# Kernel optimization log

Measured on AMD Instinct MI355X. Metric: run time of the kernel, lower is better.

The kernel has to match this reference:

```python
import jax, jax.numpy as jnp
import numpy as np

VIS_DIM, TXT_DIM, HID = 2048, 1024, 1024


def setup_inputs() -> dict:
    key = jax.random.key(0)
    ks = jax.random.split(key, 8)
    def lin(kw, kb, fan_in, fan_out):
        bound = 1.0 / np.sqrt(fan_in)
        W = jax.random.uniform(kw, (fan_out, fan_in), jnp.float32, -bound, bound)
        b = jax.random.uniform(kb, (fan_out,), jnp.float32, -bound, bound)
        return W, b
    Wv, bv = lin(ks[0], ks[1], VIS_DIM, HID)
    Wt, bt = lin(ks[2], ks[3], TXT_DIM, HID)
    Wa, ba = lin(ks[4], ks[5], HID, 1)
    return {
        "visual_features": jax.random.normal(ks[6], (128, 256, VIS_DIM), jnp.float32),
        "text_features": jax.random.normal(ks[7], (128, TXT_DIM), jnp.float32),
        "Wv": Wv, "bv": bv, "Wt": Wt, "bt": bt, "Wa": Wa, "ba": ba,
    }


def reference(visual_features, text_features, Wv, bv, Wt, bt, Wa, ba):
    # v: (B, R, H); t: (B, 1, H) broadcast over regions
    v = jnp.einsum("brd,hd->brh", visual_features, Wv) + bv
    t = (text_features @ Wt.T + bt)[:, None, :]
    combined = jnp.tanh(v + t)                       # (B, R, H)
    scores = jnp.einsum("brh,h->br", combined, Wa[0]) + ba[0]  # (B, R)
    attention_weights = jax.nn.softmax(scores, axis=1)
    attended = jnp.einsum("br,brd->bd", attention_weights, visual_features)
    return attended, attention_weights
```

## Files before the change

kernel.cpp:

```cpp
#include <hip/hip_runtime.h>
#include <hip/hip_bf16.h>

#define VIS_DIM 2048
#define TXT_DIM 1024
#define HID     1024
#define NB      128
#define NR      256
#define M_TOT   (NB*NR)

typedef __attribute__((ext_vector_type(4))) float  f32x4;
typedef __attribute__((ext_vector_type(8))) short  short8;
typedef __attribute__((ext_vector_type(4))) unsigned short u16x4;

static __device__ __forceinline__ unsigned short f2bf(float f) {
    union { __hip_bfloat16 h; unsigned short u; } c;
    c.h = __float2bfloat16(f);
    return c.u;
}

static __device__ __forceinline__ float tanh_fast(float x) {
    float xc = fminf(fmaxf(x, -15.f), 15.f);
    float e  = __expf(2.f * xc);
    return (e - 1.f) / (e + 1.f);
}

__global__ void init_ws(float* __restrict__ scores, float* __restrict__ tbuf,
                        const float* __restrict__ bt) {
    int i = blockIdx.x * 256 + threadIdx.x;
    if (i < M_TOT) scores[i] = 0.f;
    tbuf[i] = bt[i & (HID - 1)];
}

__global__ __launch_bounds__(256) void gemm_text(const float* __restrict__ text,
                                                 const float* __restrict__ Wt,
                                                 float* __restrict__ tbuf) {
    __shared__ float As[128][33];
    __shared__ float Bs[32][33];
    const int n0  = blockIdx.x * 32;
    const int k0  = blockIdx.y * 256;
    const int tid = threadIdx.x;
    const int tm  = tid >> 3;
    const int tn  = tid & 7;
    float acc[4][4] = {};
    for (int kt = 0; kt < 8; ++kt) {
        const int k = k0 + kt * 32;
        {
            int row = tid >> 1, off = (tid & 1) * 16;
            const float* src = text + row * TXT_DIM + k + off;
            #pragma unroll
            for (int j = 0; j < 4; ++j) {
                f32x4 v = *(const f32x4*)(src + j * 4);
                As[row][off + j*4 + 0] = v.x; As[row][off + j*4 + 1] = v.y;
                As[row][off + j*4 + 2] = v.z; As[row][off + j*4 + 3] = v.w;
            }
        }
        {
            int row = tid >> 3, off = (tid & 7) * 4;
            f32x4 v = *(const f32x4*)(Wt + (size_t)(n0 + row) * TXT_DIM + k + off);
            Bs[row][off + 0] = v.x; Bs[row][off + 1] = v.y;
            Bs[row][off + 2] = v.z; Bs[row][off + 3] = v.w;
        }
        __syncthreads();
        #pragma unroll
        for (int kk = 0; kk < 32; ++kk) {
            float a[4], b[4];
            #pragma unroll
            for (int i = 0; i < 4; ++i) a[i] = As[tm*4 + i][kk];
            #pragma unroll
            for (int j = 0; j < 4; ++j) b[j] = Bs[tn*4 + j][kk];
            #pragma unroll
            for (int i = 0; i < 4; ++i)
                #pragma unroll
                for (int j = 0; j < 4; ++j) acc[i][j] += a[i] * b[j];
        }
        __syncthreads();
    }
    #pragma unroll
    for (int i = 0; i < 4; ++i)
        #pragma unroll
        for (int j = 0; j < 4; ++j)
            atomicAdd(&tbuf[(tm*4 + i) * HID + n0 + tn*4 + j], acc[i][j]);
}

#define BK 32
#define NT (VIS_DIM / BK)

static __device__ __forceinline__ int tile_off(int row, int kElem) {
    return row * 64 + (((kElem >> 3) ^ ((row >> 1) & 3)) << 4);
}

__global__ __launch_bounds__(256, 2) void gemm_vis(
        const float* __restrict__ A,
        const float* __restrict__ Bv,
        const float* __restrict__ bv,
        const float* __restrict__ wa,
        const float* __restrict__ tbuf,
        float* __restrict__ scores) {
    __shared__ __align__(16) char lds[32768];

    const int wg   = blockIdx.x;
    const int xcd  = wg & 7;
    const int loc  = wg >> 3;
    const int mb   = xcd * 32 + (loc >> 3);
    const int nb   = loc & 7;
    const int brow = mb * 128;
    const int bcol = nb * 128;

    const int tid  = threadIdx.x;
    const int lane = tid & 63;
    const int wid  = tid >> 6;
    const int wr   = wid >> 1, wc = wid & 1;

    const int srow = tid >> 3;
    const int sfs  = tid & 7;
    unsigned va0 = ((unsigned)(brow + srow      ) * VIS_DIM + sfs * 4) * 4u;
    unsigned va1 = va0 + 32u * VIS_DIM * 4u;
    unsigned va2 = va0 + 64u * VIS_DIM * 4u;
    unsigned va3 = va0 + 96u * VIS_DIM * 4u;
    unsigned vb0 = ((unsigned)(bcol + srow      ) * VIS_DIM + sfs * 4) * 4u;
    unsigned vb1 = vb0 + 32u * VIS_DIM * 4u;
    unsigned vb2 = vb0 + 64u * VIS_DIM * 4u;
    unsigned vb3 = vb0 + 96u * VIS_DIM * 4u;

    int wbyte[4];
    #pragma unroll
    for (int r = 0; r < 4; ++r) {
        int row = srow + 32 * r;
        wbyte[r] = row * 64 + (((sfs >> 1) ^ ((row >> 1) & 3)) << 4) + (sfs & 1) * 8;
    }

    f32x4 sA0, sA1, sA2, sA3, sB0, sB1, sB2, sB3;
    f32x4 tA0, tA1, tA2, tA3, tB0, tB1, tB2, tB3;
    f32x4 acc[4][4] = {};

#define GLOAD_SET(dA0,dA1,dA2,dA3,dB0,dB1,dB2,dB3)                             \
    do {                                                                       \
        asm volatile("global_load_dwordx4 %0, %1, %2"                          \
                     : "=&v"(dA0) : "v"(va0), "s"(A) : "memory");              \
        asm volatile("global_load_dwordx4 %0, %1, %2"                          \
                     : "=&v"(dA1) : "v"(va1), "s"(A) : "memory");              \
        asm volatile("global_load_dwordx4 %0, %1, %2"                          \
                     : "=&v"(dA2) : "v"(va2), "s"(A) : "memory");              \
        asm volatile("global_load_dwordx4 %0, %1, %2"                          \
                     : "=&v"(dA3) : "v"(va3), "s"(A) : "memory");              \
        asm volatile("global_load_dwordx4 %0, %1, %2"                          \
                     : "=&v"(dB0) : "v"(vb0), "s"(Bv) : "memory");             \
        asm volatile("global_load_dwordx4 %0, %1, %2"                          \
                     : "=&v"(dB1) : "v"(vb1), "s"(Bv) : "memory");             \
        asm volatile("global_load_dwordx4 %0, %1, %2"                          \
                     : "=&v"(dB2) : "v"(vb2), "s"(Bv) : "memory");             \
        asm volatile("global_load_dwordx4 %0, %1, %2"                          \
                     : "=&v"(dB3) : "v"(vb3), "s"(Bv) : "memory");             \
        va0 += BK * 4; va1 += BK * 4; va2 += BK * 4; va3 += BK * 4;            \
        vb0 += BK * 4; vb1 += BK * 4; vb2 += BK * 4; vb3 += BK * 4;            \
    } while (0)

#define GLOAD_S() GLOAD_SET(sA0,sA1,sA2,sA3,sB0,sB1,sB2,sB3)
#define GLOAD_T() GLOAD_SET(tA0,tA1,tA2,tA3,tB0,tB1,tB2,tB3)

#define VWAIT(N)                                                               \
    do {                                                                       \
        __builtin_amdgcn_sched_barrier(0);                                     \
        asm volatile("s_waitcnt vmcnt(" #N ")" ::: "memory");                  \
        __builtin_amdgcn_sched_barrier(0);                                     \
    } while (0)

#define BARRIER()                                                              \
    do {                                                                       \
        __builtin_amdgcn_sched_barrier(0);                                     \
        asm volatile("s_waitcnt lgkmcnt(0)" ::: "memory");                     \
        __builtin_amdgcn_s_barrier();                                          \
        __builtin_amdgcn_sched_barrier(0);                                     \
    } while (0)

#define CVT8(dst, v0)                                                          \
    do {                                                                       \
        u16x4 t_;                                                              \
        t_.x = f2bf((v0).x); t_.y = f2bf((v0).y);                              \
        t_.z = f2bf((v0).z); t_.w = f2bf((v0).w);                              \
        dst = t_;                                                              \
    } while (0)

#define LWRITE_SET(bufbase, dA0,dA1,dA2,dA3,dB0,dB1,dB2,dB3)                   \
    do {                                                                       \
        u16x4 w_;                                                              \
        char* la = lds + (bufbase);                                            \
        char* lb = lds + (bufbase) + 8192;                                     \
        CVT8(w_, dA0); *(u16x4*)(la + wbyte[0]) = w_;                          \
        CVT8(w_, dA1); *(u16x4*)(la + wbyte[1]) = w_;                          \
        CVT8(w_, dA2); *(u16x4*)(la + wbyte[2]) = w_;                          \
        CVT8(w_, dA3); *(u16x4*)(la + wbyte[3]) = w_;                          \
        CVT8(w_, dB0); *(u16x4*)(lb + wbyte[0]) = w_;                          \
        CVT8(w_, dB1); *(u16x4*)(lb + wbyte[1]) = w_;                          \
        CVT8(w_, dB2); *(u16x4*)(lb + wbyte[2]) = w_;                          \
        CVT8(w_, dB3); *(u16x4*)(lb + wbyte[3]) = w_;                          \
    } while (0)

#define LWRITE_S(bufbase) LWRITE_SET(bufbase, sA0,sA1,sA2,sA3,sB0,sB1,sB2,sB3)
#define LWRITE_T(bufbase) LWRITE_SET(bufbase, tA0,tA1,tA2,tA3,tB0,tB1,tB2,tB3)

#define COMPUTE(bufbase)                                                       \
    do {                                                                       \
        short8 af[4], bf[4];                                                   \
        const int kk = (lane >> 4) * 8;                                        \
        const char* la = lds + (bufbase);                                      \
        const char* lb = lds + (bufbase) + 8192;                               \
        _Pragma("unroll")                                                      \
        for (int m = 0; m < 4; ++m)                                            \
            af[m] = *(const short8*)(la + tile_off(wr*64 + m*16 + (lane&15), kk)); \
        _Pragma("unroll")                                                      \
        for (int n = 0; n < 4; ++n)                                            \
            bf[n] = *(const short8*)(lb + tile_off(wc*64 + n*16 + (lane&15), kk)); \
        _Pragma("unroll")                                                      \
        for (int m = 0; m < 4; ++m)                                            \
            _Pragma("unroll")                                                  \
            for (int n = 0; n < 4; ++n)                                        \
                acc[m][n] = __builtin_amdgcn_mfma_f32_16x16x32_bf16(           \
                    af[m], bf[n], acc[m][n], 0, 0, 0);                         \
    } while (0)

    GLOAD_S();
    GLOAD_T();
    VWAIT(8);
    LWRITE_S(0);
    BARRIER();

    #pragma unroll 1
    for (int kt = 0; kt < NT - 2; kt += 2) {
        GLOAD_S();
        COMPUTE(0);
        VWAIT(8);
        LWRITE_T(16384);
        BARRIER();
        GLOAD_T();
        COMPUTE(16384);
        VWAIT(8);
        LWRITE_S(0);
        BARRIER();
    }
    COMPUTE(0);
    VWAIT(0);
    LWRITE_T(16384);
    BARRIER();
    COMPUTE(16384);
#undef GLOAD_SET
#undef GLOAD_S
#undef GLOAD_T
#undef VWAIT
#undef BARRIER
#undef CVT8
#undef LWRITE_SET
#undef LWRITE_S
#undef LWRITE_T
#undef COMPUTE

    const int b = brow >> 8;
    float wa_c[4], bvt_c[4];
    #pragma unroll
    for (int n = 0; n < 4; ++n) {
        int col = bcol + wc * 64 + n * 16 + (lane & 15);
        wa_c[n]  = wa[col];
        bvt_c[n] = bv[col] + tbuf[b * HID + col];
    }
    #pragma unroll
    for (int m = 0; m < 4; ++m) {
        float p0 = 0.f, p1 = 0.f, p2 = 0.f, p3 = 0.f;
        #pragma unroll
        for (int n = 0; n < 4; ++n) {
            f32x4 v = acc[m][n];
            p0 += wa_c[n] * tanh_fast(v.x + bvt_c[n]);
            p1 += wa_c[n] * tanh_fast(v.y + bvt_c[n]);
            p2 += wa_c[n] * tanh_fast(v.z + bvt_c[n]);
            p3 += wa_c[n] * tanh_fast(v.w + bvt_c[n]);
        }
        #pragma unroll
        for (int d = 1; d < 16; d <<= 1) {
            p0 += __shfl_xor(p0, d); p1 += __shfl_xor(p1, d);
            p2 += __shfl_xor(p2, d); p3 += __shfl_xor(p3, d);
        }
        if ((lane & 15) == 0) {
            int rowg = brow + wr * 64 + m * 16 + (lane >> 4) * 4;
            atomicAdd(&scores[rowg + 0], p0);
            atomicAdd(&scores[rowg + 1], p1);
            atomicAdd(&scores[rowg + 2], p2);
            atomicAdd(&scores[rowg + 3], p3);
        }
    }
}

__global__ __launch_bounds__(256) void attend(const float* __restrict__ visual,
                                              const float* __restrict__ scores,
                                              float* __restrict__ out) {
    const int chunk = blockIdx.x;
    const int b     = blockIdx.y;
    const int tid   = threadIdx.x;
    const int lane  = tid & 63;
    const int wv    = tid >> 6;

    __shared__ float wsm[NR];
    __shared__ float red[4];
    __shared__ f32x4 part[4][64];

    float s = scores[b * NR + tid];
    float mx = s;
    #pragma unroll
    for (int d = 1; d < 64; d <<= 1) mx = fmaxf(mx, __shfl_xor(mx, d));
    if (lane == 0) red[wv] = mx;
    __syncthreads();
    mx = fmaxf(fmaxf(red[0], red[1]), fmaxf(red[2], red[3]));
    float e = __expf(s - mx);
    float sum = e;
    #pragma unroll
    for (int d = 1; d < 64; d <<= 1) sum += __shfl_xor(sum, d);
    __syncthreads();
    if (lane == 0) red[wv] = sum;
    __syncthreads();
    sum = red[0] + red[1] + red[2] + red[3];
    float w = e * (1.f / sum);
    wsm[tid] = w;
    if (chunk == 0) out[(size_t)NB * VIS_DIM + b * NR + tid] = w;
    __syncthreads();

    const float* vb = visual + ((size_t)b * NR + wv * 64) * VIS_DIM + chunk * 256 + lane * 4;
    f32x4 acc = {0.f, 0.f, 0.f, 0.f};
    #pragma unroll
    for (int r = 0; r < 64; r += 4) {
        f32x4 v0 = *(const f32x4*)(vb + (size_t)(r + 0) * VIS_DIM);
        f32x4 v1 = *(const f32x4*)(vb + (size_t)(r + 1) * VIS_DIM);
        f32x4 v2 = *(const f32x4*)(vb + (size_t)(r + 2) * VIS_DIM);
        f32x4 v3 = *(const f32x4*)(vb + (size_t)(r + 3) * VIS_DIM);
        acc += wsm[wv * 64 + r + 0] * v0;
        acc += wsm[wv * 64 + r + 1] * v1;
        acc += wsm[wv * 64 + r + 2] * v2;
        acc += wsm[wv * 64 + r + 3] * v3;
    }
    part[wv][lane] = acc;
    __syncthreads();
    if (wv == 0) {
        f32x4 a = part[0][lane] + part[1][lane] + part[2][lane] + part[3][lane];
        *(f32x4*)(out + (size_t)b * VIS_DIM + chunk * 256 + lane * 4) = a;
    }
}

extern "C" void kernel_launch(void* const* d_in, const int* in_sizes, int n_in,
                              void* d_out, int out_size, void* d_ws, size_t ws_size,
                              hipStream_t stream) {
    (void)in_sizes; (void)n_in; (void)out_size; (void)ws_size;
    const float* visual = (const float*)d_in[0];
    const float* text   = (const float*)d_in[1];
    const float* Wv     = (const float*)d_in[2];
    const float* bv     = (const float*)d_in[3];
    const float* Wt     = (const float*)d_in[4];
    const float* bt     = (const float*)d_in[5];
    const float* Wa     = (const float*)d_in[6];

    float* out    = (float*)d_out;
    float* scores = (float*)d_ws;
    float* tbuf   = scores + M_TOT;

    init_ws  <<<512, 256, 0, stream>>>(scores, tbuf, bt);
    gemm_text<<<dim3(32, 4), 256, 0, stream>>>(text, Wt, tbuf);
    gemm_vis <<<2048, 256, 0, stream>>>(visual, Wv, bv, Wa, tbuf, scores);
    attend   <<<dim3(8, NB), 256, 0, stream>>>(visual, scores, out);
}
```

Baseline: 280.6 us.

## Use 512-thread workgroups with 8 waves per 128x128 tile in visual GEMM

```diff
diff --git a/kernel.cpp b/kernel.cpp
--- a/kernel.cpp
+++ b/kernel.cpp
@@ -89,7 +89,7 @@
     return row * 64 + (((kElem >> 3) ^ ((row >> 1) & 3)) << 4);
 }
 
-__global__ __launch_bounds__(256, 2) void gemm_vis(
+__global__ __launch_bounds__(512, 4) void gemm_vis(
         const float* __restrict__ A,
         const float* __restrict__ Bv,
         const float* __restrict__ bv,
@@ -109,54 +109,42 @@
     const int tid  = threadIdx.x;
     const int lane = tid & 63;
     const int wid  = tid >> 6;
-    const int wr   = wid >> 1, wc = wid & 1;
+    const int wr   = wid >> 2;
+    const int wc   = wid & 3;
 
     const int srow = tid >> 3;
     const int sfs  = tid & 7;
-    unsigned va0 = ((unsigned)(brow + srow      ) * VIS_DIM + sfs * 4) * 4u;
-    unsigned va1 = va0 + 32u * VIS_DIM * 4u;
-    unsigned va2 = va0 + 64u * VIS_DIM * 4u;
-    unsigned va3 = va0 + 96u * VIS_DIM * 4u;
-    unsigned vb0 = ((unsigned)(bcol + srow      ) * VIS_DIM + sfs * 4) * 4u;
-    unsigned vb1 = vb0 + 32u * VIS_DIM * 4u;
-    unsigned vb2 = vb0 + 64u * VIS_DIM * 4u;
-    unsigned vb3 = vb0 + 96u * VIS_DIM * 4u;
-
-    int wbyte[4];
-    #pragma unroll
-    for (int r = 0; r < 4; ++r) {
-        int row = srow + 32 * r;
+    unsigned va0 = ((unsigned)(brow + srow) * VIS_DIM + sfs * 4) * 4u;
+    unsigned va1 = va0 + 64u * VIS_DIM * 4u;
+    unsigned vb0 = ((unsigned)(bcol + srow) * VIS_DIM + sfs * 4) * 4u;
+    unsigned vb1 = vb0 + 64u * VIS_DIM * 4u;
+
+    int wbyte[2];
+    #pragma unroll
+    for (int r = 0; r < 2; ++r) {
+        int row = srow + 64 * r;
         wbyte[r] = row * 64 + (((sfs >> 1) ^ ((row >> 1) & 3)) << 4) + (sfs & 1) * 8;
     }
 
-    f32x4 sA0, sA1, sA2, sA3, sB0, sB1, sB2, sB3;
-    f32x4 tA0, tA1, tA2, tA3, tB0, tB1, tB2, tB3;
-    f32x4 acc[4][4] = {};
-
-#define GLOAD_SET(dA0,dA1,dA2,dA3,dB0,dB1,dB2,dB3)                             \
+    f32x4 sA0, sA1, sB0, sB1;
+    f32x4 tA0, tA1, tB0, tB1;
+    f32x4 acc[4][2] = {};
+
+#define GLOAD_SET(dA0,dA1,dB0,dB1)                                             \
     do {                                                                       \
         asm volatile("global_load_dwordx4 %0, %1, %2"                          \
                      : "=&v"(dA0) : "v"(va0), "s"(A) : "memory");              \
         asm volatile("global_load_dwordx4 %0, %1, %2"                          \
                      : "=&v"(dA1) : "v"(va1), "s"(A) : "memory");              \
         asm volatile("global_load_dwordx4 %0, %1, %2"                          \
-                     : "=&v"(dA2) : "v"(va2), "s"(A) : "memory");              \
-        asm volatile("global_load_dwordx4 %0, %1, %2"                          \
-                     : "=&v"(dA3) : "v"(va3), "s"(A) : "memory");              \
-        asm volatile("global_load_dwordx4 %0, %1, %2"                          \
                      : "=&v"(dB0) : "v"(vb0), "s"(Bv) : "memory");             \
         asm volatile("global_load_dwordx4 %0, %1, %2"                          \
                      : "=&v"(dB1) : "v"(vb1), "s"(Bv) : "memory");             \
-        asm volatile("global_load_dwordx4 %0, %1, %2"                          \
-                     : "=&v"(dB2) : "v"(vb2), "s"(Bv) : "memory");             \
-        asm volatile("global_load_dwordx4 %0, %1, %2"                          \
-                     : "=&v"(dB3) : "v"(vb3), "s"(Bv) : "memory");             \
-        va0 += BK * 4; va1 += BK * 4; va2 += BK * 4; va3 += BK * 4;            \
-        vb0 += BK * 4; vb1 += BK * 4; vb2 += BK * 4; vb3 += BK * 4;            \
-    } while (0)
-
-#define GLOAD_S() GLOAD_SET(sA0,sA1,sA2,sA3,sB0,sB1,sB2,sB3)
-#define GLOAD_T() GLOAD_SET(tA0,tA1,tA2,tA3,tB0,tB1,tB2,tB3)
+        va0 += BK * 4; va1 += BK * 4; vb0 += BK * 4; vb1 += BK * 4;            \
+    } while (0)
+
+#define GLOAD_S() GLOAD_SET(sA0,sA1,sB0,sB1)
+#define GLOAD_T() GLOAD_SET(tA0,tA1,tB0,tB1)
 
 #define VWAIT(N)                                                               \
     do {                                                                       \
@@ -181,27 +169,23 @@
         dst = t_;                                                              \
     } while (0)
 
-#define LWRITE_SET(bufbase, dA0,dA1,dA2,dA3,dB0,dB1,dB2,dB3)                   \
+#define LWRITE_SET(bufbase, dA0,dA1,dB0,dB1)                                   \
     do {                                                                       \
         u16x4 w_;                                                              \
         char* la = lds + (bufbase);                                            \
         char* lb = lds + (bufbase) + 8192;                                     \
         CVT8(w_, dA0); *(u16x4*)(la + wbyte[0]) = w_;                          \
         CVT8(w_, dA1); *(u16x4*)(la + wbyte[1]) = w_;                          \
-        CVT8(w_, dA2); *(u16x4*)(la + wbyte[2]) = w_;                          \
-        CVT8(w_, dA3); *(u16x4*)(la + wbyte[3]) = w_;                          \
         CVT8(w_, dB0); *(u16x4*)(lb + wbyte[0]) = w_;                          \
         CVT8(w_, dB1); *(u16x4*)(lb + wbyte[1]) = w_;                          \
-        CVT8(w_, dB2); *(u16x4*)(lb + wbyte[2]) = w_;                          \
-        CVT8(w_, dB3); *(u16x4*)(lb + wbyte[3]) = w_;                          \
-    } while (0)
-
-#define LWRITE_S(bufbase) LWRITE_SET(bufbase, sA0,sA1,sA2,sA3,sB0,sB1,sB2,sB3)
-#define LWRITE_T(bufbase) LWRITE_SET(bufbase, tA0,tA1,tA2,tA3,tB0,tB1,tB2,tB3)
+    } while (0)
+
+#define LWRITE_S(bufbase) LWRITE_SET(bufbase, sA0,sA1,sB0,sB1)
+#define LWRITE_T(bufbase) LWRITE_SET(bufbase, tA0,tA1,tB0,tB1)
 
 #define COMPUTE(bufbase)                                                       \
     do {                                                                       \
-        short8 af[4], bf[4];                                                   \
+        short8 af[4], bf[2];                                                   \
         const int kk = (lane >> 4) * 8;                                        \
         const char* la = lds + (bufbase);                                      \
         const char* lb = lds + (bufbase) + 8192;                               \
@@ -209,19 +193,19 @@
         for (int m = 0; m < 4; ++m)                                            \
             af[m] = *(const short8*)(la + tile_off(wr*64 + m*16 + (lane&15), kk)); \
         _Pragma("unroll")                                                      \
-        for (int n = 0; n < 4; ++n)                                            \
-            bf[n] = *(const short8*)(lb + tile_off(wc*64 + n*16 + (lane&15), kk)); \
+        for (int n = 0; n < 2; ++n)                                            \
+            bf[n] = *(const short8*)(lb + tile_off(wc*32 + n*16 + (lane&15), kk)); \
         _Pragma("unroll")                                                      \
         for (int m = 0; m < 4; ++m)                                            \
             _Pragma("unroll")                                                  \
-            for (int n = 0; n < 4; ++n)                                        \
+            for (int n = 0; n < 2; ++n)                                        \
                 acc[m][n] = __builtin_amdgcn_mfma_f32_16x16x32_bf16(           \
                     af[m], bf[n], acc[m][n], 0, 0, 0);                         \
     } while (0)
 
     GLOAD_S();
     GLOAD_T();
-    VWAIT(8);
+    VWAIT(4);
     LWRITE_S(0);
     BARRIER();
 
@@ -229,12 +213,12 @@
     for (int kt = 0; kt < NT - 2; kt += 2) {
         GLOAD_S();
         COMPUTE(0);
-        VWAIT(8);
+        VWAIT(4);
         LWRITE_T(16384);
         BARRIER();
         GLOAD_T();
         COMPUTE(16384);
-        VWAIT(8);
+        VWAIT(4);
         LWRITE_S(0);
         BARRIER();
     }
@@ -255,10 +239,10 @@
 #undef COMPUTE
 
     const int b = brow >> 8;
-    float wa_c[4], bvt_c[4];
-    #pragma unroll
-    for (int n = 0; n < 4; ++n) {
-        int col = bcol + wc * 64 + n * 16 + (lane & 15);
+    float wa_c[2], bvt_c[2];
+    #pragma unroll
+    for (int n = 0; n < 2; ++n) {
+        int col = bcol + wc * 32 + n * 16 + (lane & 15);
         wa_c[n]  = wa[col];
         bvt_c[n] = bv[col] + tbuf[b * HID + col];
     }
@@ -266,7 +250,7 @@
     for (int m = 0; m < 4; ++m) {
         float p0 = 0.f, p1 = 0.f, p2 = 0.f, p3 = 0.f;
         #pragma unroll
-        for (int n = 0; n < 4; ++n) {
+        for (int n = 0; n < 2; ++n) {
             f32x4 v = acc[m][n];
             p0 += wa_c[n] * tanh_fast(v.x + bvt_c[n]);
             p1 += wa_c[n] * tanh_fast(v.y + bvt_c[n]);
@@ -360,6 +344,6 @@
 
     init_ws  <<<512, 256, 0, stream>>>(scores, tbuf, bt);
     gemm_text<<<dim3(32, 4), 256, 0, stream>>>(text, Wt, tbuf);
-    gemm_vis <<<2048, 256, 0, stream>>>(visual, Wv, bv, Wa, tbuf, scores);
+    gemm_vis <<<2048, 512, 0, stream>>>(visual, Wv, bv, Wa, tbuf, scores);
     attend   <<<dim3(8, NB), 256, 0, stream>>>(visual, scores, out);
 }
```

Result: slower. 330.6 us (+17.8%).

## Pre-convert visual features and Wv to swizzled bf16 tiles before GEMM

Applied to the files above, without the earlier changes.

```diff
diff --git a/kernel.cpp b/kernel.cpp
--- a/kernel.cpp
+++ b/kernel.cpp
@@ -8,6 +8,12 @@
 #define NR      256
 #define M_TOT   (NB*NR)
 
+#define N_ATILES 8192
+#define N_TILES  8448
+#define TILE_B   16384
+#define WS_SCORES_OFF ((size_t)N_TILES * TILE_B)
+#define WS_NEED (WS_SCORES_OFF + 131072 + 524288)
+
 typedef __attribute__((ext_vector_type(4))) float  f32x4;
 typedef __attribute__((ext_vector_type(8))) short  short8;
 typedef __attribute__((ext_vector_type(4))) unsigned short u16x4;
@@ -29,6 +35,31 @@
     int i = blockIdx.x * 256 + threadIdx.x;
     if (i < M_TOT) scores[i] = 0.f;
     tbuf[i] = bt[i & (HID - 1)];
+}
+
+__global__ __launch_bounds__(256) void prepass(const float* __restrict__ A,
+                                               const float* __restrict__ Bv,
+                                               unsigned short* __restrict__ w16) {
+    const int t   = blockIdx.x;
+    const int tid = threadIdx.x;
+    const int mb  = (t < N_ATILES ? t : t - N_ATILES) >> 5;
+    const int kt  = t & 31;
+    const float* src = (t < N_ATILES ? A : Bv) + (size_t)mb * 128 * VIS_DIM + kt * 64;
+    unsigned short* dst = w16 + (size_t)t * (TILE_B / 2);
+    #pragma unroll
+    for (int i = 0; i < 4; ++i) {
+        int si = i * 256 + tid;
+        int row = si >> 3, slot = si & 7;
+        const float* p = src + (size_t)row * VIS_DIM + slot * 8;
+        f32x4 lo = *(const f32x4*)p;
+        f32x4 hi = *(const f32x4*)(p + 4);
+        short8 v;
+        v[0] = (short)f2bf(lo.x); v[1] = (short)f2bf(lo.y);
+        v[2] = (short)f2bf(lo.z); v[3] = (short)f2bf(lo.w);
+        v[4] = (short)f2bf(hi.x); v[5] = (short)f2bf(hi.y);
+        v[6] = (short)f2bf(hi.z); v[7] = (short)f2bf(hi.w);
+        *(short8*)(dst + row * 64 + ((slot ^ (row & 7)) << 3)) = v;
+    }
 }
 
 __global__ __launch_bounds__(256) void gemm_text(const float* __restrict__ text,
@@ -80,6 +111,106 @@
         #pragma unroll
         for (int j = 0; j < 4; ++j)
             atomicAdd(&tbuf[(tm*4 + i) * HID + n0 + tn*4 + j], acc[i][j]);
+}
+
+static __device__ __forceinline__ int toff(int row, int kElem) {
+    return row * 128 + ((((kElem >> 3) & 7) ^ (row & 7)) << 4);
+}
+
+__global__ __launch_bounds__(256, 3) void gemm_fast(
+        const unsigned short* __restrict__ w16,
+        const float* __restrict__ bv,
+        const float* __restrict__ wa,
+        const float* __restrict__ tbuf,
+        float* __restrict__ scores) {
+    __shared__ __align__(16) char lds[32768];
+
+    const int wg   = blockIdx.x;
+    const int xcd  = wg & 7;
+    const int loc  = wg >> 3;
+    const int mb   = xcd * 32 + (loc >> 3);
+    const int nb   = loc & 7;
+    const int brow = mb * 128;
+    const int bcol = nb * 128;
+
+    const int tid  = threadIdx.x;
+    const int lane = tid & 63;
+    const int wid  = tid >> 6;
+    const int wr   = wid >> 1, wc = wid & 1;
+    const int l    = lane & 15, g = lane >> 4;
+
+    const char* Abase = (const char*)w16 + (size_t)(mb * 32) * TILE_B;
+    const char* Bbase = (const char*)w16 + (size_t)(N_ATILES + nb * 32) * TILE_B;
+    const int uoff = wid * 4096;
+
+    f32x4 acc[4][4] = {};
+
+    for (int kt = 0; kt < 32; ++kt) {
+        const char* At = Abase + (size_t)kt * TILE_B;
+        const char* Bt = Bbase + (size_t)kt * TILE_B;
+        #pragma unroll
+        for (int j = 0; j < 4; ++j) {
+            const int off = uoff + j * 1024;
+            __builtin_amdgcn_global_load_lds(
+                (const __attribute__((address_space(1))) float*)(At + off + lane * 16),
+                (__attribute__((address_space(3))) float*)(lds + off), 16, 0, 0);
+            __builtin_amdgcn_global_load_lds(
+                (const __attribute__((address_space(1))) float*)(Bt + off + lane * 16),
+                (__attribute__((address_space(3))) float*)(lds + 16384 + off), 16, 0, 0);
+        }
+        __syncthreads();
+        #pragma unroll
+        for (int s = 0; s < 2; ++s) {
+            short8 af[4], bf[4];
+            const int kE = s * 32 + g * 8;
+            #pragma unroll
+            for (int m = 0; m < 4; ++m)
+                af[m] = *(const short8*)(lds + toff(wr*64 + m*16 + l, kE));
+            #pragma unroll
+            for (int n = 0; n < 4; ++n)
+                bf[n] = *(const short8*)(lds + 16384 + toff(wc*64 + n*16 + l, kE));
+            #pragma unroll
+            for (int m = 0; m < 4; ++m)
+                #pragma unroll
+                for (int n = 0; n < 4; ++n)
+                    acc[m][n] = __builtin_amdgcn_mfma_f32_16x16x32_bf16(
+                        af[m], bf[n], acc[m][n], 0, 0, 0);
+        }
+        __syncthreads();
+    }
+
+    const int b = brow >> 8;
+    float wa_c[4], bvt_c[4];
+    #pragma unroll
+    for (int n = 0; n < 4; ++n) {
+        int col = bcol + wc * 64 + n * 16 + l;
+        wa_c[n]  = wa[col];
+        bvt_c[n] = bv[col] + tbuf[b * HID + col];
+    }
+    #pragma unroll
+    for (int m = 0; m < 4; ++m) {
+        float p0 = 0.f, p1 = 0.f, p2 = 0.f, p3 = 0.f;
+        #pragma unroll
+        for (int n = 0; n < 4; ++n) {
+            f32x4 v = acc[m][n];
+            p0 += wa_c[n] * tanh_fast(v.x + bvt_c[n]);
+            p1 += wa_c[n] * tanh_fast(v.y + bvt_c[n]);
+            p2 += wa_c[n] * tanh_fast(v.z + bvt_c[n]);
+            p3 += wa_c[n] * tanh_fast(v.w + bvt_c[n]);
+        }
+        #pragma unroll
+        for (int d = 1; d < 16; d <<= 1) {
+            p0 += __shfl_xor(p0, d); p1 += __shfl_xor(p1, d);
+            p2 += __shfl_xor(p2, d); p3 += __shfl_xor(p3, d);
+        }
+        if ((lane & 15) == 0) {
+            int rowg = brow + wr * 64 + m * 16 + (lane >> 4) * 4;
+            atomicAdd(&scores[rowg + 0], p0);
+            atomicAdd(&scores[rowg + 1], p1);
+            atomicAdd(&scores[rowg + 2], p2);
+            atomicAdd(&scores[rowg + 3], p3);
+        }
+    }
 }
 
 #define BK 32
@@ -345,7 +476,7 @@
 extern "C" void kernel_launch(void* const* d_in, const int* in_sizes, int n_in,
                               void* d_out, int out_size, void* d_ws, size_t ws_size,
                               hipStream_t stream) {
-    (void)in_sizes; (void)n_in; (void)out_size; (void)ws_size;
+    (void)in_sizes; (void)n_in; (void)out_size;
     const float* visual = (const float*)d_in[0];
     const float* text   = (const float*)d_in[1];
     const float* Wv     = (const float*)d_in[2];
@@ -354,12 +485,24 @@
     const float* bt     = (const float*)d_in[5];
     const float* Wa     = (const float*)d_in[6];
 
-    float* out    = (float*)d_out;
-    float* scores = (float*)d_ws;
-    float* tbuf   = scores + M_TOT;
-
-    init_ws  <<<512, 256, 0, stream>>>(scores, tbuf, bt);
-    gemm_text<<<dim3(32, 4), 256, 0, stream>>>(text, Wt, tbuf);
-    gemm_vis <<<2048, 256, 0, stream>>>(visual, Wv, bv, Wa, tbuf, scores);
-    attend   <<<dim3(8, NB), 256, 0, stream>>>(visual, scores, out);
-}
+    float* out = (float*)d_out;
+    const bool fast = ws_size >= (size_t)WS_NEED;
+
+    if (fast) {
+        unsigned short* w16 = (unsigned short*)d_ws;
+        float* scores = (float*)((char*)d_ws + WS_SCORES_OFF);
+        float* tbuf   = scores + M_TOT;
+        prepass  <<<N_TILES, 256, 0, stream>>>(visual, Wv, w16);
+        init_ws  <<<512, 256, 0, stream>>>(scores, tbuf, bt);
+        gemm_text<<<dim3(32, 4), 256, 0, stream>>>(text, Wt, tbuf);
+        gemm_fast<<<2048, 256, 0, stream>>>(w16, bv, Wa, tbuf, scores);
+        attend   <<<dim3(8, NB), 256, 0, stream>>>(visual, scores, out);
+    } else {
+        float* scores = (float*)d_ws;
+        float* tbuf   = scores + M_TOT;
+        init_ws  <<<512, 256, 0, stream>>>(scores, tbuf, bt);
+        gemm_text<<<dim3(32, 4), 256, 0, stream>>>(text, Wt, tbuf);
+        gemm_vis <<<2048, 256, 0, stream>>>(visual, Wv, bv, Wa, tbuf, scores);
+        attend   <<<dim3(8, NB), 256, 0, stream>>>(visual, scores, out);
+    }
+}
```

Result: slower. 289.1 us (+3.0%).
